# Optimization experiments

Measured on AMD Instinct MI355X. Metric: run time of the kernel, lower is better.

## Reference

```python
import jax, jax.numpy as jnp
import numpy as np

B, CIN, C, N, K = 2, 64, 128, 8192, 16
GROUPS = C // 16
EPS = 1e-5


def lrelu(x):
    return jnp.where(x >= 0, x, 0.1 * x)


def conv1d(x, w, b):  # x:(B,Ci,N) w:(Co,Ci)
    return jnp.einsum('oc,bcn->bon', w, x) + b[None, :, None]


def conv2d(x, w, b):  # x:(B,Ci,N,K) w:(Co,Ci)
    return jnp.einsum('oc,bcnk->bonk', w, x) + b[None, :, None, None]


def groupnorm(x, gamma, beta, groups=GROUPS):
    # normalize over (C/groups, *spatial) per sample per group
    b, c = x.shape[0], x.shape[1]
    xr = x.reshape(b, groups, -1)
    mean = xr.mean(-1, keepdims=True)
    var = xr.var(-1, keepdims=True)
    xn = ((xr - mean) * jax.lax.rsqrt(var + EPS)).reshape(x.shape)
    shp = (1, c) + (1,) * (x.ndim - 2)
    return xn * gamma.reshape(shp) + beta.reshape(shp)


def knn_idx(xyz, k):  # xyz:(B,3,N) -> idx:(B,N,K)
    pts = jnp.transpose(xyz, (0, 2, 1))  # (B,N,3)
    sq = jnp.sum(pts * pts, axis=-1)  # (B,N)
    inner = jnp.einsum('bnc,bmc->bnm', pts, pts)
    d2 = sq[:, :, None] + sq[:, None, :] - 2.0 * inner  # (B,N,N)
    _, idx = jax.lax.top_k(-d2, k)
    return idx


def group(x, idx):  # x:(B,C,N) idx:(B,N,K) -> (B,C,N,K)
    b, c, n = x.shape
    k = idx.shape[-1]
    idxe = jnp.broadcast_to(idx.reshape(b, 1, n * k), (b, c, n * k))
    return jnp.take_along_axis(x, idxe, axis=2).reshape(b, c, n, k)


def reference(xyz, feat, pre_w, pre_b, wq_w, wq_b, wk_w, wk_b, wv_w, wv_b,
              pos1_w, pos1_b, pos1_g, pos1_be, pos2_w, pos2_b,
              att1_w, att1_b, att1_g, att1_be, att2_w, att2_b,
              post_w, post_b, post_g, post_be):
    idx = knn_idx(xyz, K)  # (B,N,K)
    new_feat = conv1d(feat, pre_w, pre_b)  # (B,C,N)
    rel = group(xyz, idx) - xyz[:, :, :, None]  # (B,3,N,K)
    pos = lrelu(groupnorm(conv2d(rel, pos1_w, pos1_b), pos1_g, pos1_be))
    pos = conv2d(pos, pos2_w, pos2_b)  # (B,C,N,K)
    q = conv1d(new_feat, wq_w, wq_b)
    k = group(conv1d(new_feat, wk_w, wk_b), idx)  # (B,C,N,K)
    v = group(conv1d(new_feat, wv_w, wv_b), idx)
    att = q[:, :, :, None] - k + pos
    att = lrelu(groupnorm(conv2d(att, att1_w, att1_b), att1_g, att1_be))
    att = conv2d(att, att2_w, att2_b)
    att = jax.nn.softmax(att, axis=3)
    out = jnp.sum(att * v, axis=3)  # (B,C,N)
    out = lrelu(groupnorm(conv1d(out + new_feat, post_w, post_b), post_g, post_be))
    return out


def setup_inputs():
    key = jax.random.key(0)
    ks = jax.random.split(key, 16)
    s = 0.05
    d = {
        'xyz': jax.random.normal(ks[0], (B, 3, N), jnp.float32),
        'feat': jax.random.normal(ks[1], (B, CIN, N), jnp.float32),
        'pre_w': jax.random.normal(ks[2], (C, CIN), jnp.float32) * s,
        'pre_b': jnp.zeros((C,), jnp.float32),
        'wq_w': jax.random.normal(ks[3], (C, C), jnp.float32) * s,
        'wq_b': jnp.zeros((C,), jnp.float32),
        'wk_w': jax.random.normal(ks[4], (C, C), jnp.float32) * s,
        'wk_b': jnp.zeros((C,), jnp.float32),
        'wv_w': jax.random.normal(ks[5], (C, C), jnp.float32) * s,
        'wv_b': jnp.zeros((C,), jnp.float32),
        'pos1_w': jax.random.normal(ks[6], (C, 3), jnp.float32) * s,
        'pos1_b': jnp.zeros((C,), jnp.float32),
        'pos1_g': jnp.ones((C,), jnp.float32),
        'pos1_be': jnp.zeros((C,), jnp.float32),
        'pos2_w': jax.random.normal(ks[7], (C, C), jnp.float32) * s,
        'pos2_b': jnp.zeros((C,), jnp.float32),
        'att1_w': jax.random.normal(ks[8], (C, C), jnp.float32) * s,
        'att1_b': jnp.zeros((C,), jnp.float32),
        'att1_g': jnp.ones((C,), jnp.float32),
        'att1_be': jnp.zeros((C,), jnp.float32),
        'att2_w': jax.random.normal(ks[9], (C, C), jnp.float32) * s,
        'att2_b': jnp.zeros((C,), jnp.float32),
        'post_w': jax.random.normal(ks[10], (C, C), jnp.float32) * s,
        'post_b': jnp.zeros((C,), jnp.float32),
        'post_g': jnp.ones((C,), jnp.float32),
        'post_be': jnp.zeros((C,), jnp.float32),
    }
    return d
```

## Files before the change

### kernel.cpp

```cpp
#include <hip/hip_runtime.h>
#include <hip/hip_bf16.h>

#define BB 2
#define NN 8192
#define CC 128
#define CIN_ 64
#define KK 16
#define EPSV 1e-5f

typedef __attribute__((ext_vector_type(8))) short short8;
typedef __attribute__((ext_vector_type(4))) float f32x4;

static const size_t OFF_NF   = 262144;
static const size_t OFF_OUT2 = OFF_NF  + 2097152;
static const size_t OFF_Y    = OFF_OUT2 + 2097152;
static const size_t OFF_AQB  = OFF_Y   + 16777216;
static const size_t OFF_AKB  = OFF_AQB + 1048576;
static const size_t OFF_VFB  = OFF_AKB + 1048576;
static const size_t OFF_WQ2  = OFF_VFB + 1048576;
static const size_t OFF_WK2  = OFF_WQ2 + 16384;
static const size_t OFF_PWT  = OFF_WK2 + 16384;
static const size_t OFF_W2B  = OFF_PWT + 16384;
static const size_t OFF_A2B  = OFF_W2B + 8192;
static const size_t OFF_BY   = OFF_A2B + 8192;
static const size_t OFF_RST  = OFF_BY  + 128;
static const size_t OFF_REDA = OFF_RST + 32;
static const size_t OFF_REDP = OFF_REDA + 32;
static const size_t OFF_S1   = OFF_REDP + 32;
static const size_t OFF_T1   = OFF_S1 + 256;
static const size_t OFF_S2   = OFF_T1 + 256;
static const size_t OFF_T2   = OFF_S2 + 256;
static const size_t OFF_S3   = OFF_T2 + 256;
static const size_t OFF_T3   = OFF_S3 + 256;
static const size_t OFF_PTS4 = OFF_T3 + 256;
static const size_t OFF_PTA  = OFF_PTS4 + 65536;
static const size_t OFF_PTP  = OFF_PTA + 65536;

__device__ __forceinline__ unsigned fkey_u(float d) {
  unsigned u = __float_as_uint(d);
  return (u & 0x80000000u) ? ~u : (u | 0x80000000u);
}
__device__ __forceinline__ unsigned long long shflx64(unsigned long long v, int m) {
  int lo = __shfl_xor((int)(unsigned)(v & 0xffffffffu), m, 64);
  int hi = __shfl_xor((int)(unsigned)(v >> 32), m, 64);
  return ((unsigned long long)(unsigned)hi << 32) | (unsigned)lo;
}
__device__ __forceinline__ float bf2f(unsigned short u) {
  return __uint_as_float((unsigned)u << 16);
}
__device__ __forceinline__ unsigned short f2bf(float f) {
  __hip_bfloat16 h = __float2bfloat16(f);
  unsigned short r;
  __builtin_memcpy(&r, &h, 2);
  return r;
}
__device__ __forceinline__ unsigned pack2bf(float a, float b) {
  return (unsigned)f2bf(a) | ((unsigned)f2bf(b) << 16);
}

__global__ __launch_bounds__(128) void prep_weights(
    const float* __restrict__ att1_w, const float* __restrict__ wq_w, const float* __restrict__ wk_w,
    const float* __restrict__ pos2_w, const float* __restrict__ att2_w, const float* __restrict__ post_w,
    const float* __restrict__ wq_b, const float* __restrict__ wk_b, const float* __restrict__ pos2_b,
    const float* __restrict__ att1_b,
    float* __restrict__ WQ2, float* __restrict__ WK2, __hip_bfloat16* __restrict__ W2b,
    __hip_bfloat16* __restrict__ A2b, float* __restrict__ PWT, float* __restrict__ bias_y) {
  int blk = blockIdx.x, t = threadIdx.x;
  if (blk < 128) {
    int c = blk;
    __shared__ float row[128];
    row[t] = att1_w[c * 128 + t];
    __syncthreads();
    float sq = 0.f, sk = 0.f, sp = 0.f;
    for (int m = 0; m < 128; ++m) {
      float r = row[m];
      sq = fmaf(r, wq_w[m * 128 + t], sq);
      sk = fmaf(r, wk_w[m * 128 + t], sk);
      sp = fmaf(r, pos2_w[m * 128 + t], sp);
    }
    WQ2[c * 128 + t] = sq;
    WK2[c * 128 + t] = sk;
    W2b[c * 128 + t] = __float2bfloat16(sp);
  } else if (blk == 128) {
    for (int e = t; e < 16384; e += 128) {
      int c = e >> 7, cp = e & 127;
      A2b[e] = __float2bfloat16(att2_w[e]);
      PWT[cp * 128 + c] = post_w[e];
    }
  } else {
    float s = att1_b[t];
    for (int m = 0; m < 128; ++m)
      s = fmaf(att1_w[t * 128 + m], wq_b[m] - wk_b[m] + pos2_b[m], s);
    bias_y[t] = s;
  }
}

__global__ __launch_bounds__(256) void pts4_kernel(const float* __restrict__ xyz,
                                                   float4* __restrict__ pts4) {
  int e = blockIdx.x * 256 + threadIdx.x;
  int b = e >> 13, n = e & 8191;
  const float* X = xyz + b * 3 * NN;
  float x = X[n], y = X[NN + n], z = X[2 * NN + n];
  pts4[e] = make_float4(-2.0f * x, -2.0f * y, -2.0f * z, fmaf(z, z, fmaf(y, y, x * x)));
}

#define SLOTS 96
__global__ __launch_bounds__(256) void knn_kernel(const float4* __restrict__ pts4,
                                                  int* __restrict__ idxb) {
  __shared__ unsigned long long list[16][SLOTS];
  __shared__ float chm[16][33];
  __shared__ float taus[16];
  __shared__ int cnt[16];
  int t = threadIdx.x;
  int wid = t >> 6, lane = t & 63;
  int blk = blockIdx.x;
  int b = blk >> 9;
  int q0 = (blk & 511) << 4;
  const float4* P = pts4 + b * NN;
  if (t < 16) cnt[t] = 0;
  float qsx[16], qsy[16], qsz[16];
#pragma unroll
  for (int j = 0; j < 16; ++j) {
    float4 qv = P[q0 + j];
    qsx[j] = qv.x; qsy[j] = qv.y; qsz[j] = qv.z;
  }

  for (int ch = 0; ch < 8; ++ch) {
    const float4* Pc = P + (wid << 11) + (ch << 8);
    float4 cv0 = Pc[lane];
    float4 cv1 = Pc[64 + lane];
    float4 cv2 = Pc[128 + lane];
    float4 cv3 = Pc[192 + lane];
    float c0x = -0.5f * cv0.x, c0y = -0.5f * cv0.y, c0z = -0.5f * cv0.z;
    float c1x = -0.5f * cv1.x, c1y = -0.5f * cv1.y, c1z = -0.5f * cv1.z;
    float c2x = -0.5f * cv2.x, c2y = -0.5f * cv2.y, c2z = -0.5f * cv2.z;
    float c3x = -0.5f * cv3.x, c3y = -0.5f * cv3.y, c3z = -0.5f * cv3.z;
    float mn[16];
#pragma unroll
    for (int j = 0; j < 16; ++j) {
      float d0 = fmaf(qsx[j], c0x, fmaf(qsy[j], c0y, fmaf(qsz[j], c0z, cv0.w)));
      float d1 = fmaf(qsx[j], c1x, fmaf(qsy[j], c1y, fmaf(qsz[j], c1z, cv1.w)));
      float d2 = fmaf(qsx[j], c2x, fmaf(qsy[j], c2y, fmaf(qsz[j], c2z, cv2.w)));
      float d3 = fmaf(qsx[j], c3x, fmaf(qsy[j], c3y, fmaf(qsz[j], c3z, cv3.w)));
      mn[j] = fminf(fminf(d0, d1), fminf(d2, d3));
    }
#pragma unroll
    for (int off = 32; off; off >>= 1)
#pragma unroll
      for (int j = 0; j < 16; ++j) mn[j] = fminf(mn[j], __shfl_xor(mn[j], off));
    if (lane == 0) {
#pragma unroll
      for (int j = 0; j < 16; ++j) chm[j][(wid << 3) + ch] = mn[j];
    }
  }
  __syncthreads();

  if (t < 16) {
    float v[32];
#pragma unroll
    for (int i = 0; i < 32; ++i) v[i] = chm[t][i];
    float lo = v[0], hi = v[0];
#pragma unroll
    for (int i = 1; i < 32; ++i) { lo = fminf(lo, v[i]); hi = fmaxf(hi, v[i]); }
    for (int it = 0; it < 12; ++it) {
      float mid = 0.5f * (lo + hi);
      int c = 0;
#pragma unroll
      for (int i = 0; i < 32; ++i) c += (v[i] <= mid) ? 1 : 0;
      if (c >= 16) hi = mid; else lo = mid;
    }
    taus[t] = hi;
  }
  __syncthreads();
  float tauv[16];
#pragma unroll
  for (int j = 0; j < 16; ++j) tauv[j] = taus[j];

  for (int i = 0; i < 32; ++i) {
    int ci = (wid << 11) + (i << 6) + lane;
    float4 cv = P[ci];
    float cx = -0.5f * cv.x, cy = -0.5f * cv.y, cz = -0.5f * cv.z;
#pragma unroll
    for (int j = 0; j < 16; ++j) {
      float d = fmaf(qsx[j], cx, fmaf(qsy[j], cy, fmaf(qsz[j], cz, cv.w)));
      if (d <= tauv[j]) {
        int sl = atomicAdd(&cnt[j], 1);
        if (sl < SLOTS)
          list[j][sl] = ((unsigned long long)fkey_u(d) << 32) | (unsigned)ci;
      }
    }
  }
  __syncthreads();

  for (int pp = 0; pp < 2; ++pp) {
    int qa = (wid << 2) + pp * 2, qb2 = qa + 1;
    int ca = cnt[qa]; if (ca > SLOTS) ca = SLOTS;
    int cb3 = cnt[qb2]; if (cb3 > SLOTS) cb3 = SLOTS;
    unsigned long long k0a = (lane < ca) ? list[qa][lane] : ~0ULL;
    unsigned long long k1a = (lane + 64 < ca) ? list[qa][lane + 64] : ~0ULL;
    unsigned long long k0b = (lane < cb3) ? list[qb2][lane] : ~0ULL;
    unsigned long long k1b = (lane + 64 < cb3) ? list[qb2][lane + 64] : ~0ULL;
    for (int r = 0; r < 16; ++r) {
      unsigned long long wa = (k0a < k1a) ? k0a : k1a;
      unsigned long long wb = (k0b < k1b) ? k0b : k1b;
      for (int off = 32; off; off >>= 1) {
        unsigned long long oa = shflx64(wa, off);
        unsigned long long ob = shflx64(wb, off);
        if (oa < wa) wa = oa;
        if (ob < wb) wb = ob;
      }
      if (k0a == wa) k0a = ~0ULL; else if (k1a == wa) k1a = ~0ULL;
      if (k0b == wb) k0b = ~0ULL; else if (k1b == wb) k1b = ~0ULL;
      if (lane == 0) {
        idxb[((size_t)(b * NN) + q0 + qa) * 16 + r] = (int)(wa & 0xffffffffu);
        idxb[((size_t)(b * NN) + q0 + qb2) * 16 + r] = (int)(wb & 0xffffffffu);
      }
    }
  }
}

__global__ __launch_bounds__(256) void relstats_kernel(const float* __restrict__ xyz,
                                                       const int* __restrict__ idxb,
                                                       float* __restrict__ rst) {
  int b = blockIdx.x >> 8;
  int nbase = (blockIdx.x & 255) << 5;
  const float* X = xyz + b * 3 * NN;
  float a[9];
#pragma unroll
  for (int m = 0; m < 9; ++m) a[m] = 0.f;
  for (int e = threadIdx.x; e < 512; e += 256) {
    int nn = nbase + (e >> 4);
    int kk = e & 15;
    int j = idxb[(b * NN + nn) * 16 + kk];
    float rx = X[j] - X[nn];
    float ry = X[NN + j] - X[NN + nn];
    float rz = X[2 * NN + j] - X[2 * NN + nn];
    a[0] += rx; a[1] += ry; a[2] += rz;
    a[3] = fmaf(rx, rx, a[3]); a[4] = fmaf(rx, ry, a[4]); a[5] = fmaf(rx, rz, a[5]);
    a[6] = fmaf(ry, ry, a[6]); a[7] = fmaf(ry, rz, a[7]); a[8] = fmaf(rz, rz, a[8]);
  }
  __shared__ float red[4][9];
  int lane = threadIdx.x & 63, wid = threadIdx.x >> 6;
#pragma unroll
  for (int m = 0; m < 9; ++m) {
    float v = a[m];
    for (int off = 32; off; off >>= 1) v += __shfl_xor(v, off, 64);
    if (lane == 0) red[wid][m] = v;
  }
  __syncthreads();
  if (threadIdx.x < 9) {
    float v = red[0][threadIdx.x] + red[1][threadIdx.x] + red[2][threadIdx.x] + red[3][threadIdx.x];
    atomicAdd(&rst[b * 16 + threadIdx.x], v);
  }
}

__global__ __launch_bounds__(256) void t1_kernel(const float* __restrict__ rst,
    const float* __restrict__ pos1_w, const float* __restrict__ pos1_b,
    const float* __restrict__ pos1_g, const float* __restrict__ pos1_be,
    float* __restrict__ s1, float* __restrict__ t1) {
  __shared__ float gsum[16], gsum2[16];
  int t = threadIdx.x;
  if (t < 16) { gsum[t] = 0.f; gsum2[t] = 0.f; }
  __syncthreads();
  int b = t >> 7, c = t & 127;
  const float* S = rst + b * 16;
  const float Minv = 1.0f / (float)(NN * KK);
  float mx = S[0] * Minv, my = S[1] * Minv, mz = S[2] * Minv;
  float Mxx = S[3] * Minv, Mxy = S[4] * Minv, Mxz = S[5] * Minv;
  float Myy = S[6] * Minv, Myz = S[7] * Minv, Mzz = S[8] * Minv;
  float w0 = pos1_w[c * 3], w1 = pos1_w[c * 3 + 1], w2 = pos1_w[c * 3 + 2];
  float bb = pos1_b[c];
  float wm = w0 * mx + w1 * my + w2 * mz;
  float Ey = wm + bb;
  float q = w0 * w0 * Mxx + w1 * w1 * Myy + w2 * w2 * Mzz
          + 2.f * (w0 * w1 * Mxy + w0 * w2 * Mxz + w1 * w2 * Myz);
  float Ey2 = q + 2.f * bb * wm + bb * bb;
  int g = c >> 4;
  atomicAdd(&gsum[b * 8 + g], Ey);
  atomicAdd(&gsum2[b * 8 + g], Ey2);
  __syncthreads();
  float mean = gsum[b * 8 + g] * (1.f / 16.f);
  float var = fmaxf(gsum2[b * 8 + g] * (1.f / 16.f) - mean * mean, 0.f);
  float r = rsqrtf(var + EPSV);
  float sv = pos1_g[c] * r;
  s1[t] = sv;
  t1[t] = fmaf(sv, bb, pos1_be[c] - mean * sv);
}

__global__ __launch_bounds__(256) void feat_kernel(
    const float* __restrict__ feat, const float* __restrict__ pre_w, const float* __restrict__ pre_b,
    const float* __restrict__ WQ2, const float* __restrict__ WK2,
    const float* __restrict__ wv_w, const float* __restrict__ wv_b,
    float* __restrict__ nf, __hip_bfloat16* __restrict__ AqTb,
    __hip_bfloat16* __restrict__ AkTb, __hip_bfloat16* __restrict__ vfTb) {
  int b = blockIdx.x >> 9;
  int n0 = (blockIdx.x & 511) << 4;
  __shared__ float fe[64][20];
  __shared__ float nfs[128][20];
  int t = threadIdx.x;
  for (int e = t; e < 1024; e += 256) {
    int ci = e >> 4, nn2 = e & 15;
    fe[ci][nn2] = feat[(b * 64 + ci) * NN + n0 + nn2];
  }
  __syncthreads();
  int nq = t & 3, cw = t >> 2;
  {
    float acc[2][4];
#pragma unroll
    for (int m = 0; m < 2; ++m) {
      float bv = pre_b[cw + 64 * m];
      acc[m][0] = bv; acc[m][1] = bv; acc[m][2] = bv; acc[m][3] = bv;
    }
    for (int i = 0; i < 64; ++i) {
      float4 x = *(const float4*)&fe[i][nq << 2];
      float w0 = pre_w[cw * 64 + i];
      float w1 = pre_w[(cw + 64) * 64 + i];
      acc[0][0] = fmaf(w0, x.x, acc[0][0]); acc[0][1] = fmaf(w0, x.y, acc[0][1]);
      acc[0][2] = fmaf(w0, x.z, acc[0][2]); acc[0][3] = fmaf(w0, x.w, acc[0][3]);
      acc[1][0] = fmaf(w1, x.x, acc[1][0]); acc[1][1] = fmaf(w1, x.y, acc[1][1]);
      acc[1][2] = fmaf(w1, x.z, acc[1][2]); acc[1][3] = fmaf(w1, x.w, acc[1][3]);
    }
#pragma unroll
    for (int m = 0; m < 2; ++m) {
      int c = cw + 64 * m;
      float4 v = make_float4(acc[m][0], acc[m][1], acc[m][2], acc[m][3]);
      *(float4*)&nfs[c][nq << 2] = v;
      *(float4*)&nf[(b * 128 + c) * NN + n0 + (nq << 2)] = v;
    }
  }
  __syncthreads();
  for (int s = 0; s < 3; ++s) {
    const float* Wm = (s == 0) ? WQ2 : ((s == 1) ? WK2 : wv_w);
    __hip_bfloat16* D = (s == 0) ? AqTb : ((s == 1) ? AkTb : vfTb);
    float acc[2][4];
#pragma unroll
    for (int m = 0; m < 2; ++m) {
      float bv = (s == 2) ? wv_b[cw + 64 * m] : 0.f;
      acc[m][0] = bv; acc[m][1] = bv; acc[m][2] = bv; acc[m][3] = bv;
    }
    for (int i = 0; i < 128; ++i) {
      float4 x = *(const float4*)&nfs[i][nq << 2];
      float w0 = Wm[cw * 128 + i];
      float w1 = Wm[(cw + 64) * 128 + i];
      acc[0][0] = fmaf(w0, x.x, acc[0][0]); acc[0][1] = fmaf(w0, x.y, acc[0][1]);
      acc[0][2] = fmaf(w0, x.z, acc[0][2]); acc[0][3] = fmaf(w0, x.w, acc[0][3]);
      acc[1][0] = fmaf(w1, x.x, acc[1][0]); acc[1][1] = fmaf(w1, x.y, acc[1][1]);
      acc[1][2] = fmaf(w1, x.z, acc[1][2]); acc[1][3] = fmaf(w1, x.w, acc[1][3]);
    }
#pragma unroll
    for (int m = 0; m < 2; ++m) {
      int c = cw + 64 * m;
#pragma unroll
      for (int v = 0; v < 4; ++v)
        D[(size_t)(b * NN + n0 + (nq << 2) + v) * 128 + c] = __float2bfloat16(acc[m][v]);
    }
  }
}

__global__ __launch_bounds__(256) void y_kernel_mfma(const float* __restrict__ xyz,
    const int* __restrict__ idxb, const __hip_bfloat16* __restrict__ AqTb,
    const __hip_bfloat16* __restrict__ AkTb, const __hip_bfloat16* __restrict__ W2b,
    const float* __restrict__ bias_y, const float* __restrict__ pos1_w,
    const float* __restrict__ s1, const float* __restrict__ t1,
    __hip_bfloat16* __restrict__ ybuf, float* __restrict__ partA) {
  int b = blockIdx.x >> 11;
  int pb = (blockIdx.x & 2047) * 4;
  __shared__ __align__(16) __hip_bfloat16 z_s[64][136];
  __shared__ __align__(16) __hip_bfloat16 ak_s[64][136];
  __shared__ __align__(16) float aq_s[4][128];
  __shared__ float rel_s[64][4];
  __shared__ int jj[64];
  __shared__ float gns[8], gns2[8];
  int t = threadIdx.x;
  int lane = t & 63, wid = t >> 6;
  int l15 = lane & 15, quad = lane >> 4;
  if (t < 8) { gns[t] = 0.f; gns2[t] = 0.f; }
  if (t < 64) {
    int n = pb + (t >> 4);
    int j = idxb[(b * NN + pb) * 16 + t];
    jj[t] = j;
    const float* X = xyz + b * 3 * NN;
    rel_s[t][0] = X[j] - X[n];
    rel_s[t][1] = X[NN + j] - X[NN + n];
    rel_s[t][2] = X[2 * NN + j] - X[2 * NN + n];
  }
  for (int e = t; e < 512; e += 256) {
    int pt = e >> 7, c = e & 127;
    aq_s[pt][c] = bf2f(((const unsigned short*)AqTb)[((size_t)(b * NN) + pb + pt) * 128 + c]) + bias_y[c];
  }
  __syncthreads();
  {
    int cpp = t & 63, pg = t >> 6;
    int cp0 = cpp * 2;
    float w00 = pos1_w[cp0 * 3], w01 = pos1_w[cp0 * 3 + 1], w02 = pos1_w[cp0 * 3 + 2];
    float w10 = pos1_w[cp0 * 3 + 3], w11 = pos1_w[cp0 * 3 + 4], w12 = pos1_w[cp0 * 3 + 5];
    float sa = s1[b * 128 + cp0], ta = t1[b * 128 + cp0];
    float sb = s1[b * 128 + cp0 + 1], tb = t1[b * 128 + cp0 + 1];
#pragma unroll
    for (int i = 0; i < 16; ++i) {
      int pix = pg * 16 + i;
      float rx = rel_s[pix][0], ry = rel_s[pix][1], rz = rel_s[pix][2];
      float u0 = fmaf(w02, rz, fmaf(w01, ry, w00 * rx));
      float u1 = fmaf(w12, rz, fmaf(w11, ry, w10 * rx));
      float z0 = fmaf(sa, u0, ta); z0 = (z0 >= 0.f) ? z0 : 0.1f * z0;
      float z1 = fmaf(sb, u1, tb); z1 = (z1 >= 0.f) ? z1 : 0.1f * z1;
      *(unsigned*)&z_s[pix][cp0] = pack2bf(z0, z1);
    }
  }
  for (int e = t; e < 4096; e += 256) {
    int pix = e >> 6, cpp = e & 63;
    *(unsigned*)&ak_s[pix][cpp * 2] =
        *(const unsigned*)((const unsigned short*)AkTb + ((size_t)(b * NN) + jj[pix]) * 128 + cpp * 2);
  }
  short8 afr[2][4];
#pragma unroll
  for (int m2 = 0; m2 < 2; ++m2) {
    int row = (wid * 2 + m2) * 16 + l15;
#pragma unroll
    for (int k0 = 0; k0 < 4; ++k0)
      afr[m2][k0] = *(const short8*)((const unsigned short*)W2b + row * 128 + k0 * 32 + quad * 8);
  }
  __syncthreads();
  f32x4 acc[2][4];
#pragma unroll
  for (int m2 = 0; m2 < 2; ++m2)
#pragma unroll
    for (int nt = 0; nt < 4; ++nt) acc[m2][nt] = (f32x4){0.f, 0.f, 0.f, 0.f};
#pragma unroll
  for (int k0 = 0; k0 < 4; ++k0) {
#pragma unroll
    for (int nt = 0; nt < 4; ++nt) {
      short8 bfr = *(const short8*)&z_s[nt * 16 + l15][k0 * 32 + quad * 8];
      acc[0][nt] = __builtin_amdgcn_mfma_f32_16x16x32_bf16(afr[0][k0], bfr, acc[0][nt], 0, 0, 0);
      acc[1][nt] = __builtin_amdgcn_mfma_f32_16x16x32_bf16(afr[1][k0], bfr, acc[1][nt], 0, 0, 0);
    }
  }
  float lsum[2] = {0.f, 0.f}, lsum2[2] = {0.f, 0.f};
#pragma unroll
  for (int m2 = 0; m2 < 2; ++m2) {
    int c0 = (wid * 2 + m2) * 16 + quad * 4;
#pragma unroll
    for (int nt = 0; nt < 4; ++nt) {
      int pix = nt * 16 + l15;
      ushort4 au = *(ushort4*)&ak_s[pix][c0];
      float4 aq = *(float4*)&aq_s[nt][c0];
      f32x4 a = acc[m2][nt];
      float v0 = a[0] + aq.x - bf2f(au.x);
      float v1 = a[1] + aq.y - bf2f(au.y);
      float v2 = a[2] + aq.z - bf2f(au.z);
      float v3 = a[3] + aq.w - bf2f(au.w);
      lsum[m2] += (v0 + v1) + (v2 + v3);
      lsum2[m2] += fmaf(v0, v0, fmaf(v1, v1, fmaf(v2, v2, v3 * v3)));
      ushort4 yo;
      yo.x = f2bf(v0); yo.y = f2bf(v1); yo.z = f2bf(v2); yo.w = f2bf(v3);
      *(ushort4*)&ak_s[pix][c0] = yo;
    }
  }
#pragma unroll
  for (int m2 = 0; m2 < 2; ++m2) {
    float s = lsum[m2], s2 = lsum2[m2];
    for (int msk = 1; msk < 64; msk <<= 1) {
      s += __shfl_xor(s, msk);
      s2 += __shfl_xor(s2, msk);
    }
    if (lane == 0) {
      atomicAdd(&gns[wid * 2 + m2], s);
      atomicAdd(&gns2[wid * 2 + m2], s2);
    }
  }
  __syncthreads();
  size_t ybase = ((size_t)(b * NN) + pb) * 16;
  unsigned short* yb = (unsigned short*)ybuf;
  for (int e = t; e < 4096; e += 256) {
    int pix = e >> 6, cpp = e & 63;
    *(unsigned*)(yb + (ybase + pix) * 128 + cpp * 2) = *(unsigned*)&ak_s[pix][cpp * 2];
  }
  if (t < 8) {
    partA[(size_t)t * 4096 + blockIdx.x] = gns[t];
    partA[(size_t)(8 + t) * 4096 + blockIdx.x] = gns2[t];
  }
}

__global__ __launch_bounds__(256) void gnred_kernel(const float* __restrict__ part,
                                                    float* __restrict__ red) {
  int k = blockIdx.x;
  int pb = k >> 4, idx = k & 15;
  const float* p = part + (size_t)idx * 4096 + pb * 2048;
  float s = 0.f;
  for (int i = threadIdx.x; i < 2048; i += 256) s += p[i];
  __shared__ float rs[4];
  int lane = threadIdx.x & 63, wid = threadIdx.x >> 6;
  for (int off = 32; off; off >>= 1) s += __shfl_xor(s, off);
  if (lane == 0) rs[wid] = s;
  __syncthreads();
  if (threadIdx.x == 0) red[k] = rs[0] + rs[1] + rs[2] + rs[3];
}

__global__ __launch_bounds__(256) void gnaff_kernel(const float* __restrict__ red,
    const float* __restrict__ gamma, const float* __restrict__ beta, float Minv,
    float* __restrict__ sarr, float* __restrict__ tarr) {
  int t = threadIdx.x;
  int b = t >> 7, c = t & 127, g = c >> 4;
  float S = red[b * 16 + g], S2 = red[b * 16 + 8 + g];
  float mean = S * Minv;
  float var = fmaxf(S2 * Minv - mean * mean, 0.f);
  float r = rsqrtf(var + EPSV);
  float sv = gamma[c] * r;
  sarr[t] = sv;
  tarr[t] = beta[c] - mean * sv;
}

__global__ __launch_bounds__(256) void att_out_kernel(const __hip_bfloat16* __restrict__ ybuf,
    const int* __restrict__ idxb, const float* __restrict__ s2, const float* __restrict__ t2,
    const __hip_bfloat16* __restrict__ A2b, const __hip_bfloat16* __restrict__ vfTb,
    const float* __restrict__ nf, const float* __restrict__ PWT, const float* __restrict__ post_b,
    float* __restrict__ out2, float* __restrict__ partP) {
  int b = blockIdx.x >> 11;
  int pb = (blockIdx.x & 2047) * 4;
  __shared__ __align__(16) union HS {
    unsigned short h[64][136];
    float sc[2][128][17];
  } hs;
  __shared__ __align__(16) __hip_bfloat16 v_s[64][136];
  __shared__ __align__(16) float opre[4][132];
  __shared__ int jj[64];
  __shared__ float gns[8], gns2[8];
  int t = threadIdx.x;
  int lane = t & 63, wid = t >> 6;
  int l15 = lane & 15, quad = lane >> 4;
  if (t < 8) { gns[t] = 0.f; gns2[t] = 0.f; }
  if (t < 64) jj[t] = idxb[(b * NN + pb) * 16 + t];
  __syncthreads();
  size_t ybase = ((size_t)(b * NN) + pb) * 16;
  const unsigned short* yb = (const unsigned short*)ybuf;
  {
    int cpp = t & 63, pg = t >> 6;
    int c0 = cpp * 2;
    float sa = s2[b * 128 + c0], ta = t2[b * 128 + c0];
    float sb = s2[b * 128 + c0 + 1], tb = t2[b * 128 + c0 + 1];
#pragma unroll
    for (int i = 0; i < 16; ++i) {
      int pix = pg * 16 + i;
      unsigned u = *(const unsigned*)(yb + (ybase + pix) * 128 + c0);
      float y0 = bf2f((unsigned short)(u & 0xffff));
      float y1 = bf2f((unsigned short)(u >> 16));
      float h0 = fmaf(sa, y0, ta); h0 = (h0 >= 0.f) ? h0 : 0.1f * h0;
      float h1 = fmaf(sb, y1, tb); h1 = (h1 >= 0.f) ? h1 : 0.1f * h1;
      *(unsigned*)&hs.h[pix][c0] = pack2bf(h0, h1);
    }
  }
  for (int e = t; e < 4096; e += 256) {
    int pix = e >> 6, cpp = e & 63;
    *(unsigned*)&v_s[pix][cpp * 2] =
        *(const unsigned*)((const unsigned short*)vfTb + ((size_t)(b * NN) + jj[pix]) * 128 + cpp * 2);
  }
  short8 afr[2][4];
#pragma unroll
  for (int m2 = 0; m2 < 2; ++m2) {
    int row = (wid * 2 + m2) * 16 + l15;
#pragma unroll
    for (int k0 = 0; k0 < 4; ++k0)
      afr[m2][k0] = *(const short8*)((const unsigned short*)A2b + row * 128 + k0 * 32 + quad * 8);
  }
  __syncthreads();
  f32x4 acc[2][4];
#pragma unroll
  for (int m2 = 0; m2 < 2; ++m2)
#pragma unroll
    for (int nt = 0; nt < 4; ++nt) acc[m2][nt] = (f32x4){0.f, 0.f, 0.f, 0.f};
#pragma unroll
  for (int k0 = 0; k0 < 4; ++k0) {
#pragma unroll
    for (int nt = 0; nt < 4; ++nt) {
      short8 bfr = *(const short8*)&hs.h[nt * 16 + l15][k0 * 32 + quad * 8];
      acc[0][nt] = __builtin_amdgcn_mfma_f32_16x16x32_bf16(afr[0][k0], bfr, acc[0][nt], 0, 0, 0);
      acc[1][nt] = __builtin_amdgcn_mfma_f32_16x16x32_bf16(afr[1][k0], bfr, acc[1][nt], 0, 0, 0);
    }
  }
  int pidx = t >> 7;
  int cch = t & 127;
#pragma unroll
  for (int pass = 0; pass < 2; ++pass) {
    __syncthreads();
#pragma unroll
    for (int ntl = 0; ntl < 2; ++ntl) {
      int nt = pass * 2 + ntl;
#pragma unroll
      for (int m2 = 0; m2 < 2; ++m2) {
        int cb = (wid * 2 + m2) * 16 + quad * 4;
        f32x4 a = acc[m2][nt];
#pragma unroll
        for (int r = 0; r < 4; ++r) hs.sc[ntl][cb + r][l15] = a[r];
      }
    }
    __syncthreads();
    {
      int p = pass * 2 + pidx;
      float nfv = nf[(size_t)(b * 128 + cch) * NN + pb + p];
      const float* srow = hs.sc[pidx][cch];
      float sv[16];
#pragma unroll
      for (int k = 0; k < 16; ++k) sv[k] = srow[k];
      float mx = sv[0];
#pragma unroll
      for (int k = 1; k < 16; ++k) mx = fmaxf(mx, sv[k]);
      float sm = 0.f, dot = 0.f;
#pragma unroll
      for (int k = 0; k < 16; ++k) {
        float e = __expf(sv[k] - mx);
        sm += e;
        float vv = bf2f(*(const unsigned short*)&v_s[p * 16 + k][cch]);
        dot = fmaf(e, vv, dot);
      }
      opre[p][cch] = dot / sm + nfv;
    }
  }
  __syncthreads();
  {
    int c = t & 127, g = t >> 7;
    float a0 = post_b[c], a1 = a0;
    for (int cp = 0; cp < 128; ++cp) {
      float w = PWT[cp * 128 + c];
      a0 = fmaf(w, opre[g * 2][cp], a0);
      a1 = fmaf(w, opre[g * 2 + 1][cp], a1);
    }
    out2[(size_t)(b * 128 + c) * NN + pb + g * 2] = a0;
    out2[(size_t)(b * 128 + c) * NN + pb + g * 2 + 1] = a1;
    atomicAdd(&gns[c >> 4], a0 + a1);
    atomicAdd(&gns2[c >> 4], fmaf(a0, a0, a1 * a1));
  }
  __syncthreads();
  if (t < 8) {
    partP[(size_t)t * 4096 + blockIdx.x] = gns[t];
    partP[(size_t)(8 + t) * 4096 + blockIdx.x] = gns2[t];
  }
}

__global__ __launch_bounds__(256) void final_kernel(const float* __restrict__ out2,
    const float* __restrict__ s3, const float* __restrict__ t3, float* __restrict__ out) {
  int e = blockIdx.x * 256 + threadIdx.x;
  int c = (e >> 13) & 127, b = e >> 20;
  float v = fmaf(s3[b * 128 + c], out2[e], t3[b * 128 + c]);
  out[e] = (v >= 0.f) ? v : 0.1f * v;
}

extern "C" void kernel_launch(void* const* d_in, const int* in_sizes, int n_in,
                              void* d_out, int out_size, void* d_ws, size_t ws_size,
                              hipStream_t stream) {
  (void)in_sizes; (void)n_in; (void)out_size; (void)ws_size;
  const float* xyz     = (const float*)d_in[0];
  const float* feat    = (const float*)d_in[1];
  const float* pre_w   = (const float*)d_in[2];
  const float* pre_b   = (const float*)d_in[3];
  const float* wq_w    = (const float*)d_in[4];
  const float* wq_b    = (const float*)d_in[5];
  const float* wk_w    = (const float*)d_in[6];
  const float* wk_b    = (const float*)d_in[7];
  const float* wv_w    = (const float*)d_in[8];
  const float* wv_b    = (const float*)d_in[9];
  const float* pos1_w  = (const float*)d_in[10];
  const float* pos1_b  = (const float*)d_in[11];
  const float* pos1_g  = (const float*)d_in[12];
  const float* pos1_be = (const float*)d_in[13];
  const float* pos2_w  = (const float*)d_in[14];
  const float* pos2_b  = (const float*)d_in[15];
  const float* att1_w  = (const float*)d_in[16];
  const float* att1_b  = (const float*)d_in[17];
  const float* att1_g  = (const float*)d_in[18];
  const float* att1_be = (const float*)d_in[19];
  const float* att2_w  = (const float*)d_in[20];
  const float* post_w  = (const float*)d_in[22];
  const float* post_b  = (const float*)d_in[23];
  const float* post_g  = (const float*)d_in[24];
  const float* post_be = (const float*)d_in[25];

  float* W = (float*)d_ws;
  int* idxb = (int*)d_ws;
  float* nf   = W + OFF_NF;
  float* out2 = W + OFF_OUT2;
  __hip_bfloat16* ybuf = (__hip_bfloat16*)(W + OFF_Y);
  __hip_bfloat16* AqTb = (__hip_bfloat16*)(W + OFF_AQB);
  __hip_bfloat16* AkTb = (__hip_bfloat16*)(W + OFF_AKB);
  __hip_bfloat16* vfTb = (__hip_bfloat16*)(W + OFF_VFB);
  float* WQ2  = W + OFF_WQ2;
  float* WK2  = W + OFF_WK2;
  float* PWT  = W + OFF_PWT;
  __hip_bfloat16* W2b = (__hip_bfloat16*)(W + OFF_W2B);
  __hip_bfloat16* A2b = (__hip_bfloat16*)(W + OFF_A2B);
  float* BY   = W + OFF_BY;
  float* RST  = W + OFF_RST;
  float* REDA = W + OFF_REDA;
  float* REDP = W + OFF_REDP;
  float* S1 = W + OFF_S1; float* T1 = W + OFF_T1;
  float* S2 = W + OFF_S2; float* T2 = W + OFF_T2;
  float* S3 = W + OFF_S3; float* T3 = W + OFF_T3;
  float4* PTS4 = (float4*)(W + OFF_PTS4);
  float* PARTA = W + OFF_PTA;
  float* PARTP = W + OFF_PTP;

  hipMemsetAsync(RST, 0, 32 * sizeof(float), stream);

  prep_weights<<<130, 128, 0, stream>>>(att1_w, wq_w, wk_w, pos2_w, att2_w, post_w,
                                        wq_b, wk_b, pos2_b, att1_b,
                                        WQ2, WK2, W2b, A2b, PWT, BY);
  pts4_kernel<<<64, 256, 0, stream>>>(xyz, PTS4);
  knn_kernel<<<1024, 256, 0, stream>>>(PTS4, idxb);
  relstats_kernel<<<512, 256, 0, stream>>>(xyz, idxb, RST);
  t1_kernel<<<1, 256, 0, stream>>>(RST, pos1_w, pos1_b, pos1_g, pos1_be, S1, T1);
  feat_kernel<<<1024, 256, 0, stream>>>(feat, pre_w, pre_b, WQ2, WK2, wv_w, wv_b,
                                        nf, AqTb, AkTb, vfTb);
  y_kernel_mfma<<<4096, 256, 0, stream>>>(xyz, idxb, AqTb, AkTb, W2b, BY, pos1_w, S1, T1, ybuf, PARTA);
  gnred_kernel<<<32, 256, 0, stream>>>(PARTA, REDA);
  gnaff_kernel<<<1, 256, 0, stream>>>(REDA, att1_g, att1_be, 1.0f / 2097152.0f, S2, T2);
  att_out_kernel<<<4096, 256, 0, stream>>>(ybuf, idxb, S2, T2, A2b, vfTb, nf, PWT, post_b, out2, PARTP);
  gnred_kernel<<<32, 256, 0, stream>>>(PARTP, REDP);
  gnaff_kernel<<<1, 256, 0, stream>>>(REDP, post_g, post_be, 1.0f / 131072.0f, S3, T3);
  final_kernel<<<8192, 256, 0, stream>>>(out2, S3, T3, (float*)d_out);
}
```

Measured before the change: 402.1 us.

## Fuse kNN and feature projection kernels into one interleaved launch

Merges the kNN selection kernel and the feature projection kernel into a single launch. Even blocks do kNN and odd blocks do the feature GEMMs, with shared memory overlaid through a union. The independent work can overlap on the GPU, and one launch is saved. The kNN chunk-minimum pass is also restructured: each lane now owns one query and scans 64 candidates serially instead of each lane handling candidates across 16 queries with full-wave shuffles. The fused kernel's register and LDS footprint is the larger of the two, which may lower occupancy.

Result: slower. 462.4 us (+15.0%).

```diff
diff --git a/kernel.cpp b/kernel.cpp
--- a/kernel.cpp
+++ b/kernel.cpp
@@ -105,115 +105,181 @@
 }
 
 #define SLOTS 96
-__global__ __launch_bounds__(256) void knn_kernel(const float4* __restrict__ pts4,
-                                                  int* __restrict__ idxb) {
-  __shared__ unsigned long long list[16][SLOTS];
-  __shared__ float chm[16][33];
-  __shared__ float taus[16];
-  __shared__ int cnt[16];
+__global__ __launch_bounds__(256) void fused_kf_kernel(
+    const float4* __restrict__ pts4, int* __restrict__ idxb,
+    const float* __restrict__ feat, const float* __restrict__ pre_w, const float* __restrict__ pre_b,
+    const float* __restrict__ WQ2, const float* __restrict__ WK2,
+    const float* __restrict__ wv_w, const float* __restrict__ wv_b,
+    float* __restrict__ nf, __hip_bfloat16* __restrict__ AqTb,
+    __hip_bfloat16* __restrict__ AkTb, __hip_bfloat16* __restrict__ vfTb) {
+  __shared__ __align__(16) union FusedLDS {
+    struct { float fe[64][20]; float nfs[128][20]; } f;
+    struct { unsigned long long list[16][SLOTS]; float chm[16][33];
+             float taus[16]; int cnt[16]; } k;
+  } L;
   int t = threadIdx.x;
-  int wid = t >> 6, lane = t & 63;
-  int blk = blockIdx.x;
-  int b = blk >> 9;
-  int q0 = (blk & 511) << 4;
-  const float4* P = pts4 + b * NN;
-  if (t < 16) cnt[t] = 0;
-  float qsx[16], qsy[16], qsz[16];
-#pragma unroll
-  for (int j = 0; j < 16; ++j) {
-    float4 qv = P[q0 + j];
-    qsx[j] = qv.x; qsy[j] = qv.y; qsz[j] = qv.z;
-  }
-
-  for (int ch = 0; ch < 8; ++ch) {
-    const float4* Pc = P + (wid << 11) + (ch << 8);
-    float4 cv0 = Pc[lane];
-    float4 cv1 = Pc[64 + lane];
-    float4 cv2 = Pc[128 + lane];
-    float4 cv3 = Pc[192 + lane];
-    float c0x = -0.5f * cv0.x, c0y = -0.5f * cv0.y, c0z = -0.5f * cv0.z;
-    float c1x = -0.5f * cv1.x, c1y = -0.5f * cv1.y, c1z = -0.5f * cv1.z;
-    float c2x = -0.5f * cv2.x, c2y = -0.5f * cv2.y, c2z = -0.5f * cv2.z;
-    float c3x = -0.5f * cv3.x, c3y = -0.5f * cv3.y, c3z = -0.5f * cv3.z;
-    float mn[16];
-#pragma unroll
-    for (int j = 0; j < 16; ++j) {
-      float d0 = fmaf(qsx[j], c0x, fmaf(qsy[j], c0y, fmaf(qsz[j], c0z, cv0.w)));
-      float d1 = fmaf(qsx[j], c1x, fmaf(qsy[j], c1y, fmaf(qsz[j], c1z, cv1.w)));
-      float d2 = fmaf(qsx[j], c2x, fmaf(qsy[j], c2y, fmaf(qsz[j], c2z, cv2.w)));
-      float d3 = fmaf(qsx[j], c3x, fmaf(qsy[j], c3y, fmaf(qsz[j], c3z, cv3.w)));
-      mn[j] = fminf(fminf(d0, d1), fminf(d2, d3));
-    }
-#pragma unroll
-    for (int off = 32; off; off >>= 1)
-#pragma unroll
-      for (int j = 0; j < 16; ++j) mn[j] = fminf(mn[j], __shfl_xor(mn[j], off));
-    if (lane == 0) {
-#pragma unroll
-      for (int j = 0; j < 16; ++j) chm[j][(wid << 3) + ch] = mn[j];
-    }
-  }
-  __syncthreads();
-
-  if (t < 16) {
-    float v[32];
-#pragma unroll
-    for (int i = 0; i < 32; ++i) v[i] = chm[t][i];
-    float lo = v[0], hi = v[0];
-#pragma unroll
-    for (int i = 1; i < 32; ++i) { lo = fminf(lo, v[i]); hi = fmaxf(hi, v[i]); }
-    for (int it = 0; it < 12; ++it) {
-      float mid = 0.5f * (lo + hi);
-      int c = 0;
-#pragma unroll
-      for (int i = 0; i < 32; ++i) c += (v[i] <= mid) ? 1 : 0;
-      if (c >= 16) hi = mid; else lo = mid;
-    }
-    taus[t] = hi;
-  }
-  __syncthreads();
-  float tauv[16];
-#pragma unroll
-  for (int j = 0; j < 16; ++j) tauv[j] = taus[j];
-
-  for (int i = 0; i < 32; ++i) {
-    int ci = (wid << 11) + (i << 6) + lane;
-    float4 cv = P[ci];
-    float cx = -0.5f * cv.x, cy = -0.5f * cv.y, cz = -0.5f * cv.z;
-#pragma unroll
-    for (int j = 0; j < 16; ++j) {
-      float d = fmaf(qsx[j], cx, fmaf(qsy[j], cy, fmaf(qsz[j], cz, cv.w)));
-      if (d <= tauv[j]) {
-        int sl = atomicAdd(&cnt[j], 1);
-        if (sl < SLOTS)
-          list[j][sl] = ((unsigned long long)fkey_u(d) << 32) | (unsigned)ci;
-      }
-    }
-  }
-  __syncthreads();
-
-  for (int pp = 0; pp < 2; ++pp) {
-    int qa = (wid << 2) + pp * 2, qb2 = qa + 1;
-    int ca = cnt[qa]; if (ca > SLOTS) ca = SLOTS;
-    int cb3 = cnt[qb2]; if (cb3 > SLOTS) cb3 = SLOTS;
-    unsigned long long k0a = (lane < ca) ? list[qa][lane] : ~0ULL;
-    unsigned long long k1a = (lane + 64 < ca) ? list[qa][lane + 64] : ~0ULL;
-    unsigned long long k0b = (lane < cb3) ? list[qb2][lane] : ~0ULL;
-    unsigned long long k1b = (lane + 64 < cb3) ? list[qb2][lane + 64] : ~0ULL;
-    for (int r = 0; r < 16; ++r) {
-      unsigned long long wa = (k0a < k1a) ? k0a : k1a;
-      unsigned long long wb = (k0b < k1b) ? k0b : k1b;
-      for (int off = 32; off; off >>= 1) {
-        unsigned long long oa = shflx64(wa, off);
-        unsigned long long ob = shflx64(wb, off);
-        if (oa < wa) wa = oa;
-        if (ob < wb) wb = ob;
-      }
-      if (k0a == wa) k0a = ~0ULL; else if (k1a == wa) k1a = ~0ULL;
-      if (k0b == wb) k0b = ~0ULL; else if (k1b == wb) k1b = ~0ULL;
-      if (lane == 0) {
-        idxb[((size_t)(b * NN) + q0 + qa) * 16 + r] = (int)(wa & 0xffffffffu);
-        idxb[((size_t)(b * NN) + q0 + qb2) * 16 + r] = (int)(wb & 0xffffffffu);
+
+  if ((blockIdx.x & 1) == 0) {
+    int kb = blockIdx.x >> 1;
+    int wid = t >> 6, lane = t & 63;
+    int b = kb >> 9;
+    int q0 = (kb & 511) << 4;
+    const float4* P = pts4 + b * NN;
+    if (t < 16) L.k.cnt[t] = 0;
+
+    {
+      int qq = lane & 15;
+      float4 qv4 = P[q0 + qq];
+      float qxr = -0.5f * qv4.x, qyr = -0.5f * qv4.y, qzr = -0.5f * qv4.z;
+      int sl = lane >> 4;
+      for (int ch = 0; ch < 8; ++ch) {
+        const float4* Pc = P + (wid << 11) + (ch << 8) + (sl << 6);
+        float mm = 3.4e38f;
+        for (int i = 0; i < 64; i += 4) {
+          float4 c0 = Pc[i], c1 = Pc[i + 1], c2 = Pc[i + 2], c3 = Pc[i + 3];
+          float d0 = fmaf(qxr, c0.x, fmaf(qyr, c0.y, fmaf(qzr, c0.z, c0.w)));
+          float d1 = fmaf(qxr, c1.x, fmaf(qyr, c1.y, fmaf(qzr, c1.z, c1.w)));
+          float d2 = fmaf(qxr, c2.x, fmaf(qyr, c2.y, fmaf(qzr, c2.z, c2.w)));
+          float d3 = fmaf(qxr, c3.x, fmaf(qyr, c3.y, fmaf(qzr, c3.z, c3.w)));
+          mm = fminf(mm, fminf(fminf(d0, d1), fminf(d2, d3)));
+        }
+        mm = fminf(mm, __shfl_xor(mm, 16));
+        mm = fminf(mm, __shfl_xor(mm, 32));
+        if (lane < 16) L.k.chm[lane][(wid << 3) + ch] = mm;
+      }
+    }
+    __syncthreads();
+
+    if (t < 16) {
+      float v[32];
+#pragma unroll
+      for (int i = 0; i < 32; ++i) v[i] = L.k.chm[t][i];
+      float lo = v[0], hi = v[0];
+#pragma unroll
+      for (int i = 1; i < 32; ++i) { lo = fminf(lo, v[i]); hi = fmaxf(hi, v[i]); }
+      for (int it = 0; it < 12; ++it) {
+        float mid = 0.5f * (lo + hi);
+        int c = 0;
+#pragma unroll
+        for (int i = 0; i < 32; ++i) c += (v[i] <= mid) ? 1 : 0;
+        if (c >= 16) hi = mid; else lo = mid;
+      }
+      L.k.taus[t] = hi;
+    }
+    __syncthreads();
+
+    {
+      float qtx[16], qty[16], qtz[16], tauv[16];
+#pragma unroll
+      for (int j = 0; j < 16; ++j) {
+        float4 qv = P[q0 + j];
+        qtx[j] = -0.5f * qv.x; qty[j] = -0.5f * qv.y; qtz[j] = -0.5f * qv.z;
+        tauv[j] = L.k.taus[j];
+      }
+      int wid2 = t >> 6, lane2 = t & 63;
+      for (int i = 0; i < 32; ++i) {
+        int ci = (wid2 << 11) + (i << 6) + lane2;
+        float4 cv = P[ci];
+#pragma unroll
+        for (int j = 0; j < 16; ++j) {
+          float d = fmaf(qtx[j], cv.x, fmaf(qty[j], cv.y, fmaf(qtz[j], cv.z, cv.w)));
+          if (d <= tauv[j]) {
+            int sl2 = atomicAdd(&L.k.cnt[j], 1);
+            if (sl2 < SLOTS)
+              L.k.list[j][sl2] = ((unsigned long long)fkey_u(d) << 32) | (unsigned)ci;
+          }
+        }
+      }
+    }
+    __syncthreads();
+
+    {
+      int wid2 = t >> 6, lane2 = t & 63;
+      for (int pp = 0; pp < 2; ++pp) {
+        int qa = (wid2 << 2) + pp * 2, qb2 = qa + 1;
+        int ca = L.k.cnt[qa]; if (ca > SLOTS) ca = SLOTS;
+        int cb3 = L.k.cnt[qb2]; if (cb3 > SLOTS) cb3 = SLOTS;
+        unsigned long long k0a = (lane2 < ca) ? L.k.list[qa][lane2] : ~0ULL;
+        unsigned long long k1a = (lane2 + 64 < ca) ? L.k.list[qa][lane2 + 64] : ~0ULL;
+        unsigned long long k0b = (lane2 < cb3) ? L.k.list[qb2][lane2] : ~0ULL;
+        unsigned long long k1b = (lane2 + 64 < cb3) ? L.k.list[qb2][lane2 + 64] : ~0ULL;
+        for (int r = 0; r < 16; ++r) {
+          unsigned long long wa = (k0a < k1a) ? k0a : k1a;
+          unsigned long long wb = (k0b < k1b) ? k0b : k1b;
+          for (int off = 32; off; off >>= 1) {
+            unsigned long long oa = shflx64(wa, off);
+            unsigned long long ob = shflx64(wb, off);
+            if (oa < wa) wa = oa;
+            if (ob < wb) wb = ob;
+          }
+          if (k0a == wa) k0a = ~0ULL; else if (k1a == wa) k1a = ~0ULL;
+          if (k0b == wb) k0b = ~0ULL; else if (k1b == wb) k1b = ~0ULL;
+          if (lane2 == 0) {
+            idxb[((size_t)(b * NN) + q0 + qa) * 16 + r] = (int)(wa & 0xffffffffu);
+            idxb[((size_t)(b * NN) + q0 + qb2) * 16 + r] = (int)(wb & 0xffffffffu);
+          }
+        }
+      }
+    }
+  } else {
+    int fb = blockIdx.x >> 1;
+    int b = fb >> 9;
+    int n0 = (fb & 511) << 4;
+    for (int e = t; e < 1024; e += 256) {
+      int ci = e >> 4, nn2 = e & 15;
+      L.f.fe[ci][nn2] = feat[(b * 64 + ci) * NN + n0 + nn2];
+    }
+    __syncthreads();
+    int nq = t & 3, cw = t >> 2;
+    {
+      float acc[2][4];
+#pragma unroll
+      for (int m = 0; m < 2; ++m) {
+        float bv = pre_b[cw + 64 * m];
+        acc[m][0] = bv; acc[m][1] = bv; acc[m][2] = bv; acc[m][3] = bv;
+      }
+      for (int i = 0; i < 64; ++i) {
+        float4 x = *(const float4*)&L.f.fe[i][nq << 2];
+        float w0 = pre_w[cw * 64 + i];
+        float w1 = pre_w[(cw + 64) * 64 + i];
+        acc[0][0] = fmaf(w0, x.x, acc[0][0]); acc[0][1] = fmaf(w0, x.y, acc[0][1]);
+        acc[0][2] = fmaf(w0, x.z, acc[0][2]); acc[0][3] = fmaf(w0, x.w, acc[0][3]);
+        acc[1][0] = fmaf(w1, x.x, acc[1][0]); acc[1][1] = fmaf(w1, x.y, acc[1][1]);
+        acc[1][2] = fmaf(w1, x.z, acc[1][2]); acc[1][3] = fmaf(w1, x.w, acc[1][3]);
+      }
+#pragma unroll
+      for (int m = 0; m < 2; ++m) {
+        int c = cw + 64 * m;
+        float4 v = make_float4(acc[m][0], acc[m][1], acc[m][2], acc[m][3]);
+        *(float4*)&L.f.nfs[c][nq << 2] = v;
+        *(float4*)&nf[(b * 128 + c) * NN + n0 + (nq << 2)] = v;
+      }
+    }
+    __syncthreads();
+    for (int s = 0; s < 3; ++s) {
+      const float* Wm = (s == 0) ? WQ2 : ((s == 1) ? WK2 : wv_w);
+      __hip_bfloat16* D = (s == 0) ? AqTb : ((s == 1) ? AkTb : vfTb);
+      float acc[2][4];
+#pragma unroll
+      for (int m = 0; m < 2; ++m) {
+        float bv = (s == 2) ? wv_b[cw + 64 * m] : 0.f;
+        acc[m][0] = bv; acc[m][1] = bv; acc[m][2] = bv; acc[m][3] = bv;
+      }
+      for (int i = 0; i < 128; ++i) {
+        float4 x = *(const float4*)&L.f.nfs[i][nq << 2];
+        float w0 = Wm[cw * 128 + i];
+        float w1 = Wm[(cw + 64) * 128 + i];
+        acc[0][0] = fmaf(w0, x.x, acc[0][0]); acc[0][1] = fmaf(w0, x.y, acc[0][1]);
+        acc[0][2] = fmaf(w0, x.z, acc[0][2]); acc[0][3] = fmaf(w0, x.w, acc[0][3]);
+        acc[1][0] = fmaf(w1, x.x, acc[1][0]); acc[1][1] = fmaf(w1, x.y, acc[1][1]);
+        acc[1][2] = fmaf(w1, x.z, acc[1][2]); acc[1][3] = fmaf(w1, x.w, acc[1][3]);
+      }
+#pragma unroll
+      for (int m = 0; m < 2; ++m) {
+        int c = cw + 64 * m;
+#pragma unroll
+        for (int v = 0; v < 4; ++v)
+          D[(size_t)(b * NN + n0 + (nq << 2) + v) * 128 + c] = __float2bfloat16(acc[m][v]);
       }
     }
   }
@@ -285,76 +351,6 @@
   float sv = pos1_g[c] * r;
   s1[t] = sv;
   t1[t] = fmaf(sv, bb, pos1_be[c] - mean * sv);
-}
-
-__global__ __launch_bounds__(256) void feat_kernel(
-    const float* __restrict__ feat, const float* __restrict__ pre_w, const float* __restrict__ pre_b,
-    const float* __restrict__ WQ2, const float* __restrict__ WK2,
-    const float* __restrict__ wv_w, const float* __restrict__ wv_b,
-    float* __restrict__ nf, __hip_bfloat16* __restrict__ AqTb,
-    __hip_bfloat16* __restrict__ AkTb, __hip_bfloat16* __restrict__ vfTb) {
-  int b = blockIdx.x >> 9;
-  int n0 = (blockIdx.x & 511) << 4;
-  __shared__ float fe[64][20];
-  __shared__ float nfs[128][20];
-  int t = threadIdx.x;
-  for (int e = t; e < 1024; e += 256) {
-    int ci = e >> 4, nn2 = e & 15;
-    fe[ci][nn2] = feat[(b * 64 + ci) * NN + n0 + nn2];
-  }
-  __syncthreads();
-  int nq = t & 3, cw = t >> 2;
-  {
-    float acc[2][4];
-#pragma unroll
-    for (int m = 0; m < 2; ++m) {
-      float bv = pre_b[cw + 64 * m];
-      acc[m][0] = bv; acc[m][1] = bv; acc[m][2] = bv; acc[m][3] = bv;
-    }
-    for (int i = 0; i < 64; ++i) {
-      float4 x = *(const float4*)&fe[i][nq << 2];
-      float w0 = pre_w[cw * 64 + i];
-      float w1 = pre_w[(cw + 64) * 64 + i];
-      acc[0][0] = fmaf(w0, x.x, acc[0][0]); acc[0][1] = fmaf(w0, x.y, acc[0][1]);
-      acc[0][2] = fmaf(w0, x.z, acc[0][2]); acc[0][3] = fmaf(w0, x.w, acc[0][3]);
-      acc[1][0] = fmaf(w1, x.x, acc[1][0]); acc[1][1] = fmaf(w1, x.y, acc[1][1]);
-      acc[1][2] = fmaf(w1, x.z, acc[1][2]); acc[1][3] = fmaf(w1, x.w, acc[1][3]);
-    }
-#pragma unroll
-    for (int m = 0; m < 2; ++m) {
-      int c = cw + 64 * m;
-      float4 v = make_float4(acc[m][0], acc[m][1], acc[m][2], acc[m][3]);
-      *(float4*)&nfs[c][nq << 2] = v;
-      *(float4*)&nf[(b * 128 + c) * NN + n0 + (nq << 2)] = v;
-    }
-  }
-  __syncthreads();
-  for (int s = 0; s < 3; ++s) {
-    const float* Wm = (s == 0) ? WQ2 : ((s == 1) ? WK2 : wv_w);
-    __hip_bfloat16* D = (s == 0) ? AqTb : ((s == 1) ? AkTb : vfTb);
-    float acc[2][4];
-#pragma unroll
-    for (int m = 0; m < 2; ++m) {
-      float bv = (s == 2) ? wv_b[cw + 64 * m] : 0.f;
-      acc[m][0] = bv; acc[m][1] = bv; acc[m][2] = bv; acc[m][3] = bv;
-    }
-    for (int i = 0; i < 128; ++i) {
-      float4 x = *(const float4*)&nfs[i][nq << 2];
-      float w0 = Wm[cw * 128 + i];
-      float w1 = Wm[(cw + 64) * 128 + i];
-      acc[0][0] = fmaf(w0, x.x, acc[0][0]); acc[0][1] = fmaf(w0, x.y, acc[0][1]);
-      acc[0][2] = fmaf(w0, x.z, acc[0][2]); acc[0][3] = fmaf(w0, x.w, acc[0][3]);
-      acc[1][0] = fmaf(w1, x.x, acc[1][0]); acc[1][1] = fmaf(w1, x.y, acc[1][1]);
-      acc[1][2] = fmaf(w1, x.z, acc[1][2]); acc[1][3] = fmaf(w1, x.w, acc[1][3]);
-    }
-#pragma unroll
-    for (int m = 0; m < 2; ++m) {
-      int c = cw + 64 * m;
-#pragma unroll
-      for (int v = 0; v < 4; ++v)
-        D[(size_t)(b * NN + n0 + (nq << 2) + v) * 128 + c] = __float2bfloat16(acc[m][v]);
-    }
-  }
 }
 
 __global__ __launch_bounds__(256) void y_kernel_mfma(const float* __restrict__ xyz,
@@ -704,11 +700,11 @@
                                         wq_b, wk_b, pos2_b, att1_b,
                                         WQ2, WK2, W2b, A2b, PWT, BY);
   pts4_kernel<<<64, 256, 0, stream>>>(xyz, PTS4);
-  knn_kernel<<<1024, 256, 0, stream>>>(PTS4, idxb);
+  fused_kf_kernel<<<2048, 256, 0, stream>>>(PTS4, idxb,
+                                            feat, pre_w, pre_b, WQ2, WK2, wv_w, wv_b,
+                                            nf, AqTb, AkTb, vfTb);
   relstats_kernel<<<512, 256, 0, stream>>>(xyz, idxb, RST);
   t1_kernel<<<1, 256, 0, stream>>>(RST, pos1_w, pos1_b, pos1_g, pos1_be, S1, T1);
-  feat_kernel<<<1024, 256, 0, stream>>>(feat, pre_w, pre_b, WQ2, WK2, wv_w, wv_b,
-                                        nf, AqTb, AkTb, vfTb);
   y_kernel_mfma<<<4096, 256, 0, stream>>>(xyz, idxb, AqTb, AkTb, W2b, BY, pos1_w, S1, T1, ybuf, PARTA);
   gnred_kernel<<<32, 256, 0, stream>>>(PARTA, REDA);
   gnaff_kernel<<<1, 256, 0, stream>>>(REDA, att1_g, att1_be, 1.0f / 2097152.0f, S2, T2);
```
